# Performance work log

Measured on AMD Instinct MI355X. Metric: run time of the kernel, lower is better.

Reference implementation:

```python
import jax, jax.numpy as jnp
import numpy as np

B, L, C = 8, 3136, 192
HEADS, HEAD_CH = 3, 64
EPS = 1e-5


def _dwconv(x, w, s):
    # depthwise 3x3 conv, SAME padding; w: [3,3,1,C], feature_group_count=C
    return jax.lax.conv_general_dilated(
        x, w, (s, s), 'SAME',
        dimension_numbers=('NHWC', 'HWIO', 'NHWC'),
        feature_group_count=x.shape[-1])


def _proj(x, dw, scale, bias, mean, var, pw, s):
    # depthwise conv -> BN (inference, running stats) -> 1x1 pointwise conv
    h = _dwconv(x, dw, s)
    h = (h - mean) * jax.lax.rsqrt(var + EPS) * scale + bias
    return jax.lax.conv_general_dilated(
        h, pw, (1, 1), 'SAME',
        dimension_numbers=('NHWC', 'HWIO', 'NHWC'))


def setup_inputs() -> dict:
    key = jax.random.key(0)
    ks = jax.random.split(key, 7)
    d = {'x': jax.random.normal(ks[0], (B, L, C), jnp.float32)}
    for i, p in enumerate(['q', 'k', 'v']):
        d[p + '_dw'] = jax.random.normal(ks[i + 1], (3, 3, 1, C), jnp.float32) * 0.1
        d[p + '_scale'] = jnp.ones((C,), jnp.float32)
        d[p + '_bias'] = jnp.zeros((C,), jnp.float32)
        d[p + '_mean'] = jnp.zeros((C,), jnp.float32)
        d[p + '_var'] = jnp.ones((C,), jnp.float32)
        d[p + '_pw'] = jax.random.normal(ks[i + 4], (1, 1, C, HEADS * HEAD_CH), jnp.float32) * 0.05
    d['is_training'] = 0  # inference: BN uses running averages
    return d


def reference(x, q_dw, q_scale, q_bias, q_mean, q_var, q_pw,
              k_dw, k_scale, k_bias, k_mean, k_var, k_pw,
              v_dw, v_scale, v_bias, v_mean, v_var, v_pw,
              is_training):
    S = int(np.ceil(np.sqrt(L)))  # 56; L is a perfect square, so no token padding
    xi = x.reshape(B, S, S, C)
    q = _proj(xi, q_dw, q_scale, q_bias, q_mean, q_var, q_pw, 1)  # [B,56,56,192]
    k = _proj(xi, k_dw, k_scale, k_bias, k_mean, k_var, k_pw, 2)  # [B,28,28,192]
    v = _proj(xi, v_dw, v_scale, v_bias, v_mean, v_var, v_pw, 2)  # [B,28,28,192]
    q = q.reshape(B, -1, HEADS, HEAD_CH) / jnp.sqrt(jnp.float32(HEAD_CH))
    k = k.reshape(B, -1, HEADS, HEAD_CH)
    v = v.reshape(B, -1, HEADS, HEAD_CH)
    attn = jax.nn.softmax(jnp.einsum('bqhd,bkhd->bhqk', q, k), axis=-1)
    o = jnp.einsum('bhqk,bkhd->bqhd', attn, v)
    # num_heads*head_ch == out_ch -> plain head merge, no output projection
    return o.reshape(B, L, HEADS * HEAD_CH)
```

## Files before the change

### kernel.cpp

```cpp
#include <hip/hip_runtime.h>
#include <cmath>

#define EPS_BN 1e-5f

typedef __bf16 bf16;
typedef __bf16 bf16x4 __attribute__((ext_vector_type(4)));
typedef __bf16 bf16x8 __attribute__((ext_vector_type(8)));
typedef float  f32x4  __attribute__((ext_vector_type(4)));

__device__ __forceinline__ void dma16(const bf16* g, bf16* l) {
    __builtin_amdgcn_global_load_lds(
        (const __attribute__((address_space(1))) void*)g,
        (__attribute__((address_space(3))) void*)l, 16, 0, 0);
}

__device__ __forceinline__ float exp2_hw(float x) {
    float r;
    asm("v_exp_f32 %0, %1" : "=v"(r) : "v"(x));
    return r;
}

__global__ __launch_bounds__(256) void conv_all_kernel(
    const float* __restrict__ x,
    const float* __restrict__ qdw, const float* __restrict__ qscale,
    const float* __restrict__ qbias, const float* __restrict__ qmean,
    const float* __restrict__ qvar,
    const float* __restrict__ kdw, const float* __restrict__ kscale,
    const float* __restrict__ kbias, const float* __restrict__ kmean,
    const float* __restrict__ kvar,
    const float* __restrict__ vdw, const float* __restrict__ vscale,
    const float* __restrict__ vbias, const float* __restrict__ vmean,
    const float* __restrict__ vvar,
    const float* __restrict__ qpw, const float* __restrict__ kpw,
    const float* __restrict__ vpw,
    bf16* __restrict__ qhi, bf16* __restrict__ qlo,
    bf16* __restrict__ khi, bf16* __restrict__ klo,
    bf16* __restrict__ vhi, bf16* __restrict__ vlo,
    bf16* __restrict__ wt) {
    const int WW = 56, C = 192;
    int bid = blockIdx.x;

    if (bid < 4704) {
        int idx = bid * 256 + threadIdx.x;
        int p  = idx / 48;
        int c4 = (idx - p * 48) * 4;
        int b  = p / 3136;
        int rem = p - b * 3136;
        int oy = rem / 56;
        int ox = rem - oy * 56;
        const float* xb = x + (size_t)b * 3136 * C;

        float4 sc = *(const float4*)&qscale[c4];
        float4 vr = *(const float4*)&qvar[c4];
        float4 bi = *(const float4*)&qbias[c4];
        float4 mn = *(const float4*)&qmean[c4];
        float aA[4] = {sc.x * rsqrtf(vr.x + EPS_BN), sc.y * rsqrtf(vr.y + EPS_BN),
                       sc.z * rsqrtf(vr.z + EPS_BN), sc.w * rsqrtf(vr.w + EPS_BN)};
        float aB[4] = {bi.x - mn.x * aA[0], bi.y - mn.y * aA[1],
                       bi.z - mn.z * aA[2], bi.w - mn.w * aA[3]};
        float s[4] = {0.f, 0.f, 0.f, 0.f};
#pragma unroll
        for (int ky = 0; ky < 3; ky++) {
            int iy = oy + ky - 1;
            bool yok = (iy >= 0) && (iy < 56);
#pragma unroll
            for (int kx = 0; kx < 3; kx++) {
                int ix = ox + kx - 1;
                if (yok && ix >= 0 && ix < WW) {
                    float4 xv = *(const float4*)&xb[((size_t)iy * WW + ix) * C + c4];
                    float4 wv = *(const float4*)&qdw[(ky * 3 + kx) * C + c4];
                    s[0] += xv.x * wv.x; s[1] += xv.y * wv.y;
                    s[2] += xv.z * wv.z; s[3] += xv.w * wv.w;
                }
            }
        }
        bf16x4 hv, lv;
#pragma unroll
        for (int j = 0; j < 4; j++) {
            float av = s[j] * aA[j] + aB[j];
            bf16 hh = (bf16)av;
            hv[j] = hh;
            lv[j] = (bf16)(av - (float)hh);
        }
        *(bf16x4*)&qhi[(size_t)p * C + c4] = hv;
        *(bf16x4*)&qlo[(size_t)p * C + c4] = lv;
    } else if (bid < 5880) {
        int idx = (bid - 4704) * 256 + threadIdx.x;
        int p  = idx / 48;
        int c4 = (idx - p * 48) * 4;
        int b  = p / 784;
        int rem = p - b * 784;
        int oy = rem / 28;
        int ox = rem - oy * 28;
        const float* xb = x + (size_t)b * 3136 * C;

        float ks[4] = {0.f, 0.f, 0.f, 0.f};
        float vs[4] = {0.f, 0.f, 0.f, 0.f};
#pragma unroll
        for (int ky = 0; ky < 3; ky++) {
            int iy = oy * 2 + ky;
            bool yok = iy < 56;
#pragma unroll
            for (int kx = 0; kx < 3; kx++) {
                int ix = ox * 2 + kx;
                if (yok && ix < WW) {
                    float4 xv = *(const float4*)&xb[((size_t)iy * WW + ix) * C + c4];
                    float4 kw = *(const float4*)&kdw[(ky * 3 + kx) * C + c4];
                    float4 vw = *(const float4*)&vdw[(ky * 3 + kx) * C + c4];
                    ks[0] += xv.x * kw.x; ks[1] += xv.y * kw.y;
                    ks[2] += xv.z * kw.z; ks[3] += xv.w * kw.w;
                    vs[0] += xv.x * vw.x; vs[1] += xv.y * vw.y;
                    vs[2] += xv.z * vw.z; vs[3] += xv.w * vw.w;
                }
            }
        }
        float4 ksc = *(const float4*)&kscale[c4];
        float4 kvr = *(const float4*)&kvar[c4];
        float4 kbi = *(const float4*)&kbias[c4];
        float4 kmn = *(const float4*)&kmean[c4];
        float4 vsc = *(const float4*)&vscale[c4];
        float4 vvr = *(const float4*)&vvar[c4];
        float4 vbi = *(const float4*)&vbias[c4];
        float4 vmn = *(const float4*)&vmean[c4];
        float kA[4] = {ksc.x * rsqrtf(kvr.x + EPS_BN), ksc.y * rsqrtf(kvr.y + EPS_BN),
                       ksc.z * rsqrtf(kvr.z + EPS_BN), ksc.w * rsqrtf(kvr.w + EPS_BN)};
        float kB[4] = {kbi.x - kmn.x * kA[0], kbi.y - kmn.y * kA[1],
                       kbi.z - kmn.z * kA[2], kbi.w - kmn.w * kA[3]};
        float vA[4] = {vsc.x * rsqrtf(vvr.x + EPS_BN), vsc.y * rsqrtf(vvr.y + EPS_BN),
                       vsc.z * rsqrtf(vvr.z + EPS_BN), vsc.w * rsqrtf(vvr.w + EPS_BN)};
        float vB[4] = {vbi.x - vmn.x * vA[0], vbi.y - vmn.y * vA[1],
                       vbi.z - vmn.z * vA[2], vbi.w - vmn.w * vA[3]};
        bf16x4 kh, kl, vh, vl;
#pragma unroll
        for (int j = 0; j < 4; j++) {
            float kf = ks[j] * kA[j] + kB[j];
            float vf = vs[j] * vA[j] + vB[j];
            bf16 h1 = (bf16)kf; kh[j] = h1; kl[j] = (bf16)(kf - (float)h1);
            bf16 h2 = (bf16)vf; vh[j] = h2; vl[j] = (bf16)(vf - (float)h2);
        }
        *(bf16x4*)&khi[(size_t)p * C + c4] = kh;
        *(bf16x4*)&klo[(size_t)p * C + c4] = kl;
        *(bf16x4*)&vhi[(size_t)p * C + c4] = vh;
        *(bf16x4*)&vlo[(size_t)p * C + c4] = vl;
    } else {
        int idx = (bid - 5880) * 256 + threadIdx.x;
        if (idx < 3 * 36864) {
            int mat = idx / 36864, r = idx % 36864;
            int n = r / 192, k = r - n * 192;
            const float* src = (mat == 0) ? qpw : (mat == 1) ? kpw : vpw;
            wt[idx] = (bf16)src[k * 192 + n];
        }
    }
}

__global__ __launch_bounds__(256) void gemm_all_kernel(
    const bf16* __restrict__ qhi, const bf16* __restrict__ qlo,
    const bf16* __restrict__ khi, const bf16* __restrict__ klo,
    const bf16* __restrict__ vhi, const bf16* __restrict__ vlo,
    const bf16* __restrict__ wt,
    bf16* __restrict__ qbuf, bf16* __restrict__ kbuf, bf16* __restrict__ vtbuf) {
    __shared__ bf16 Ws[96][200];
    int t = threadIdx.x;
    int bid = blockIdx.x;

    int mode, mt, nh;
    const bf16 *Ahi, *Alo, *Wsrc;
    if (bid < 784)      { mode = 0; mt = bid >> 1;         nh = bid & 1;
                          Ahi = qhi; Alo = qlo; Wsrc = wt; }
    else if (bid < 980) { mode = 1; int r = bid - 784; mt = r >> 1; nh = r & 1;
                          Ahi = khi; Alo = klo; Wsrc = wt + 36864; }
    else                { mode = 2; int r = bid - 980; mt = r >> 1; nh = r & 1;
                          Ahi = vhi; Alo = vlo; Wsrc = wt + 73728; }
    int n0 = nh * 96;

#pragma unroll
    for (int it = 0; it < 9; it++) {
        int idx = it * 256 + t;
        int n = idx / 24, ck = idx - n * 24;
        *(uint4*)&Ws[n][ck * 8] = *(const uint4*)&Wsrc[(size_t)(n0 + n) * 192 + ck * 8];
    }
    __syncthreads();

    int lane = t & 63, wid = t >> 6;
    int l16 = lane & 15, quad = lane >> 4;
    int wrow = wid * 16;
    int m0 = mt * 64;

    f32x4 acc[6];
#pragma unroll
    for (int n = 0; n < 6; n++) acc[n] = f32x4{0.f, 0.f, 0.f, 0.f};

    const bf16* arh = Ahi + (size_t)(m0 + wrow + l16) * 192;
    const bf16* arl = Alo + (size_t)(m0 + wrow + l16) * 192;

    if (mode == 2) {
#pragma unroll
        for (int kc = 0; kc < 6; kc++) {
            bf16x8 ah = *(const bf16x8*)(arh + kc * 32 + quad * 8);
            bf16x8 al = *(const bf16x8*)(arl + kc * 32 + quad * 8);
#pragma unroll
            for (int n = 0; n < 6; n++) {
                bf16x8 bfr = *(const bf16x8*)&Ws[n * 16 + l16][kc * 32 + quad * 8];
                acc[n] = __builtin_amdgcn_mfma_f32_16x16x32_bf16(bfr, al, acc[n], 0, 0, 0);
                acc[n] = __builtin_amdgcn_mfma_f32_16x16x32_bf16(bfr, ah, acc[n], 0, 0, 0);
            }
        }
        int row = m0 + wrow + l16;
        int bb  = row / 784;
        int loc = row - bb * 784;
        bf16* vbase = vtbuf + (size_t)bb * 3 * 64 * 784 + loc;
#pragma unroll
        for (int n = 0; n < 6; n++)
#pragma unroll
            for (int reg = 0; reg < 4; reg++) {
                int col = n0 + n * 16 + quad * 4 + reg;
                int hh = col >> 6, d = col & 63;
                vbase[((size_t)hh * 64 + d) * 784] = (bf16)acc[n][reg];
            }
    } else {
#pragma unroll
        for (int kc = 0; kc < 6; kc++) {
            bf16x8 ah = *(const bf16x8*)(arh + kc * 32 + quad * 8);
            bf16x8 al = *(const bf16x8*)(arl + kc * 32 + quad * 8);
#pragma unroll
            for (int n = 0; n < 6; n++) {
                bf16x8 bfr = *(const bf16x8*)&Ws[n * 16 + l16][kc * 32 + quad * 8];
                acc[n] = __builtin_amdgcn_mfma_f32_16x16x32_bf16(al, bfr, acc[n], 0, 0, 0);
                acc[n] = __builtin_amdgcn_mfma_f32_16x16x32_bf16(ah, bfr, acc[n], 0, 0, 0);
            }
        }
        bf16* outp = (mode == 0) ? qbuf : kbuf;
        const float s = (mode == 0) ? 0.18033688f : 1.0f;
#pragma unroll
        for (int reg = 0; reg < 4; reg++) {
            size_t row = m0 + wrow + quad * 4 + reg;
#pragma unroll
            for (int n = 0; n < 6; n++)
                outp[row * 192 + n0 + n * 16 + l16] = (bf16)(acc[n][reg] * s);
        }
    }
}

__global__ __launch_bounds__(512)
__attribute__((amdgpu_waves_per_eu(4, 4)))
void attn3_kernel(const bf16* __restrict__ qb,
                  const bf16* __restrict__ kb,
                  const bf16* __restrict__ vtb,
                  float* __restrict__ out) {
    const int LQ = 3136, LK = 784, C = 192;
    int qt = blockIdx.x, h = blockIdx.y, b = blockIdx.z;

    __shared__ bf16 Ks[2][7168];
    __shared__ bf16 Vts[8192];
    __shared__ bf16 Ps[8192];

    int t    = threadIdx.x;
    int lane = t & 63;
    int wid  = t >> 6;
    int l16  = lane & 15;
    int quad = lane >> 4;
    int wrow = wid * 16;
    int l7   = l16 & 7;
    int qh   = quad >> 1;

    const bf16* kbase  = kb + (size_t)b * LK * C + h * 64;
    const bf16* vtbase = vtb + ((size_t)(b * 3 + h)) * 64 * LK;

    const bf16* ksrc = kbase + (lane >> 3) * C + (((lane & 7) ^ (lane >> 3)) * 8);

    int voff[2];
#pragma unroll
    for (int i = 0; i < 2; i++) {
        int s = wid + 8 * i;
        int j = s * 64 + lane;
        int row = j >> 4;
        int l = (j & 15) ^ (row & 7);
        voff[i] = row * LK + l * 8;
    }

    for (int s = wid; s < 14; s += 8)
        dma16(ksrc + s * 8 * C, &Ks[0][s * 512]);

    bf16x8 qfrag[2];
    {
        const bf16* qrow = qb + ((size_t)b * LQ + qt * 128 + wrow + l16) * C + h * 64;
        qfrag[0] = *(const bf16x8*)(qrow + quad * 8);
        qfrag[1] = *(const bf16x8*)(qrow + 32 + quad * 8);
    }
    bool qvalid = (qt < 24) || (wid < 4);

    int kA0 = l16 * 64 + (((quad    ) ^ l7) * 8);
    int kA1 = l16 * 64 + (((quad + 4) ^ l7) * 8);

    int prow   = (wrow + l16) * 64;
    int pwbase = prow + (quad & 1) * 4;

    float m_run = -INFINITY, l_run = 0.f;
    f32x4 o_acc[4];
#pragma unroll
    for (int dt = 0; dt < 4; dt++) o_acc[dt] = f32x4{0.f, 0.f, 0.f, 0.f};

    __syncthreads();

    for (int c = 0; c < 7; c++) {
        const int cur = c & 1, nxt = cur ^ 1;
        const int j0 = c * 112;

#pragma unroll
        for (int i = 0; i < 2; i++)
            dma16(vtbase + j0 + voff[i], Vts + (wid + 8 * i) * 512);
        __builtin_amdgcn_sched_barrier(0);

        if (c < 6) {
            const bf16* kn = ksrc + (size_t)(c + 1) * 112 * C;
            for (int s = wid; s < 14; s += 8)
                dma16(kn + s * 8 * C, &Ks[nxt][s * 512]);
        }
        __builtin_amdgcn_sched_barrier(0);

        f32x4 st[7];
#pragma unroll
        for (int kb7 = 0; kb7 < 7; kb7++) st[kb7] = f32x4{0.f, 0.f, 0.f, 0.f};
#pragma unroll
        for (int kk = 0; kk < 2; kk++) {
            int kA = (kk == 0) ? kA0 : kA1;
#pragma unroll
            for (int kb7 = 0; kb7 < 7; kb7++) {
                bf16x8 afrag = *(const bf16x8*)&Ks[cur][kb7 * 1024 + kA];
                st[kb7] = __builtin_amdgcn_mfma_f32_16x16x32_bf16(afrag, qfrag[kk], st[kb7], 0, 0, 0);
            }
        }

        float mx = -INFINITY;
#pragma unroll
        for (int kb7 = 0; kb7 < 7; kb7++)
#pragma unroll
            for (int r = 0; r < 4; r++) mx = fmaxf(mx, st[kb7][r]);
        mx = fmaxf(mx, __shfl_xor(mx, 16, 64));
        mx = fmaxf(mx, __shfl_xor(mx, 32, 64));

        bool defer = __all(mx - m_run <= 8.0f);
        float m_new = defer ? m_run : fmaxf(m_run, mx);

        float rs = 0.f;
        bf16x4 pk[7];
#pragma unroll
        for (int kb7 = 0; kb7 < 7; kb7++) {
            bf16x4 pv;
#pragma unroll
            for (int r = 0; r < 4; r++) {
                float p = exp2_hw(st[kb7][r] - m_new);
                rs += p;
                pv[r] = (bf16)p;
            }
            pk[kb7] = pv;
        }
        rs += __shfl_xor(rs, 16, 64);
        rs += __shfl_xor(rs, 32, 64);
        if (defer) {
            l_run += rs;
        } else {
            float alpha = exp2_hw(m_run - m_new);
            l_run = l_run * alpha + rs;
            m_run = m_new;
#pragma unroll
            for (int dt = 0; dt < 4; dt++)
#pragma unroll
                for (int r = 0; r < 4; r++) o_acc[dt][r] *= alpha;
        }

#pragma unroll
        for (int kb = 0; kb < 4; kb++)
            *(bf16x4*)&Ps[pwbase + (((kb * 2 + qh) ^ l7) * 8)] = pk[kb];

        if (c < 6) {
            if (wid < 6) asm volatile("s_waitcnt vmcnt(2)" ::: "memory");
            else         asm volatile("s_waitcnt vmcnt(1)" ::: "memory");
        } else {
            asm volatile("s_waitcnt vmcnt(0)" ::: "memory");
        }
        __builtin_amdgcn_s_barrier();
        __builtin_amdgcn_sched_barrier(0);

#pragma unroll
        for (int kk = 0; kk < 2; kk++) {
            bf16x8 pfrag = *(const bf16x8*)&Ps[prow + (((kk * 4 + quad) ^ l7) * 8)];
#pragma unroll
            for (int dt = 0; dt < 4; dt++) {
                bf16x8 vfrag = *(const bf16x8*)&Vts[(dt * 16 + l16) * 128
                                                   + (((kk * 4 + quad) ^ l7) * 8)];
                o_acc[dt] = __builtin_amdgcn_mfma_f32_16x16x32_bf16(vfrag, pfrag, o_acc[dt], 0, 0, 0);
            }
        }

#pragma unroll
        for (int kb = 0; kb < 3; kb++)
            *(bf16x4*)&Ps[pwbase + (((kb * 2 + qh) ^ l7) * 8)] = pk[4 + kb];
        {
            bf16x4 zv = {(bf16)0.f, (bf16)0.f, (bf16)0.f, (bf16)0.f};
            *(bf16x4*)&Ps[pwbase + (((6 + qh) ^ l7) * 8)] = zv;
        }

#pragma unroll
        for (int kk = 2; kk < 4; kk++) {
            bf16x8 pfrag = *(const bf16x8*)&Ps[prow + ((((kk - 2) * 4 + quad) ^ l7) * 8)];
#pragma unroll
            for (int dt = 0; dt < 4; dt++) {
                bf16x8 vfrag = *(const bf16x8*)&Vts[(dt * 16 + l16) * 128
                                                   + (((kk * 4 + quad) ^ l7) * 8)];
                o_acc[dt] = __builtin_amdgcn_mfma_f32_16x16x32_bf16(vfrag, pfrag, o_acc[dt], 0, 0, 0);
            }
        }

        __syncthreads();
    }

    if (qvalid) {
        float invl = 1.f / l_run;
        float* ob = out + ((size_t)b * LQ + qt * 128 + wrow + l16) * C + h * 64;
#pragma unroll
        for (int dt = 0; dt < 4; dt++) {
            float4 v4 = {o_acc[dt][0] * invl, o_acc[dt][1] * invl,
                         o_acc[dt][2] * invl, o_acc[dt][3] * invl};
            *(float4*)(ob + dt * 16 + quad * 4) = v4;
        }
    }
}

extern "C" void kernel_launch(void* const* d_in, const int* in_sizes, int n_in,
                              void* d_out, int out_size, void* d_ws, size_t ws_size,
                              hipStream_t stream) {
    const float* x = (const float*)d_in[0];

    const float* q_dw = (const float*)d_in[1];
    const float* q_scale = (const float*)d_in[2];
    const float* q_bias = (const float*)d_in[3];
    const float* q_mean = (const float*)d_in[4];
    const float* q_var = (const float*)d_in[5];
    const float* q_pw = (const float*)d_in[6];

    const float* k_dw = (const float*)d_in[7];
    const float* k_scale = (const float*)d_in[8];
    const float* k_bias = (const float*)d_in[9];
    const float* k_mean = (const float*)d_in[10];
    const float* k_var = (const float*)d_in[11];
    const float* k_pw = (const float*)d_in[12];

    const float* v_dw = (const float*)d_in[13];
    const float* v_scale = (const float*)d_in[14];
    const float* v_bias = (const float*)d_in[15];
    const float* v_mean = (const float*)d_in[16];
    const float* v_var = (const float*)d_in[17];
    const float* v_pw = (const float*)d_in[18];

    float* out = (float*)d_out;

    char* ws = (char*)d_ws;
    bf16* qhi = (bf16*)(ws);
    bf16* qlo = (bf16*)(ws + 9633792);
    bf16* khi = (bf16*)(ws + 19267584);
    bf16* klo = (bf16*)(ws + 21676032);
    bf16* vhi = (bf16*)(ws + 24084480);
    bf16* vlo = (bf16*)(ws + 26492928);
    bf16* qbuf = (bf16*)(ws + 28901376);
    bf16* kbuf = (bf16*)(ws + 38535168);
    bf16* vtbuf = (bf16*)(ws + 40943616);
    bf16* wt = (bf16*)(ws + 43352064);

    conv_all_kernel<<<6312, 256, 0, stream>>>(
        x,
        q_dw, q_scale, q_bias, q_mean, q_var,
        k_dw, k_scale, k_bias, k_mean, k_var,
        v_dw, v_scale, v_bias, v_mean, v_var,
        q_pw, k_pw, v_pw,
        qhi, qlo, khi, klo, vhi, vlo, wt);

    gemm_all_kernel<<<1176, 256, 0, stream>>>(
        qhi, qlo, khi, klo, vhi, vlo, wt, qbuf, kbuf, vtbuf);

    attn3_kernel<<<dim3(25, 3, 8), 512, 0, stream>>>(qbuf, kbuf, vtbuf, out);
}
```

Measured before the change: 174.2 us.

## Fuse Q depthwise conv, BN and pointwise GEMM into one kernel

The Q path's depthwise conv and BN now run in registers and feed the MFMA pointwise projection directly. The qhi/qlo intermediate buffers, about 19 MB written and read back, are no longer materialized. The fused kernel reads weights straight from global memory rather than LDS and uses only 392 blocks, so occupancy is low and the kernel may be latency bound. The conv and GEMM kernels shrink to the K/V work only.

```diff
diff --git a/kernel.cpp b/kernel.cpp
--- a/kernel.cpp
+++ b/kernel.cpp
@@ -22,9 +22,6 @@
 
 __global__ __launch_bounds__(256) void conv_all_kernel(
     const float* __restrict__ x,
-    const float* __restrict__ qdw, const float* __restrict__ qscale,
-    const float* __restrict__ qbias, const float* __restrict__ qmean,
-    const float* __restrict__ qvar,
     const float* __restrict__ kdw, const float* __restrict__ kscale,
     const float* __restrict__ kbias, const float* __restrict__ kmean,
     const float* __restrict__ kvar,
@@ -33,59 +30,14 @@
     const float* __restrict__ vvar,
     const float* __restrict__ qpw, const float* __restrict__ kpw,
     const float* __restrict__ vpw,
-    bf16* __restrict__ qhi, bf16* __restrict__ qlo,
     bf16* __restrict__ khi, bf16* __restrict__ klo,
     bf16* __restrict__ vhi, bf16* __restrict__ vlo,
     bf16* __restrict__ wt) {
     const int WW = 56, C = 192;
     int bid = blockIdx.x;
 
-    if (bid < 4704) {
+    if (bid < 1176) {
         int idx = bid * 256 + threadIdx.x;
-        int p  = idx / 48;
-        int c4 = (idx - p * 48) * 4;
-        int b  = p / 3136;
-        int rem = p - b * 3136;
-        int oy = rem / 56;
-        int ox = rem - oy * 56;
-        const float* xb = x + (size_t)b * 3136 * C;
-
-        float4 sc = *(const float4*)&qscale[c4];
-        float4 vr = *(const float4*)&qvar[c4];
-        float4 bi = *(const float4*)&qbias[c4];
-        float4 mn = *(const float4*)&qmean[c4];
-        float aA[4] = {sc.x * rsqrtf(vr.x + EPS_BN), sc.y * rsqrtf(vr.y + EPS_BN),
-                       sc.z * rsqrtf(vr.z + EPS_BN), sc.w * rsqrtf(vr.w + EPS_BN)};
-        float aB[4] = {bi.x - mn.x * aA[0], bi.y - mn.y * aA[1],
-                       bi.z - mn.z * aA[2], bi.w - mn.w * aA[3]};
-        float s[4] = {0.f, 0.f, 0.f, 0.f};
-#pragma unroll
-        for (int ky = 0; ky < 3; ky++) {
-            int iy = oy + ky - 1;
-            bool yok = (iy >= 0) && (iy < 56);
-#pragma unroll
-            for (int kx = 0; kx < 3; kx++) {
-                int ix = ox + kx - 1;
-                if (yok && ix >= 0 && ix < WW) {
-                    float4 xv = *(const float4*)&xb[((size_t)iy * WW + ix) * C + c4];
-                    float4 wv = *(const float4*)&qdw[(ky * 3 + kx) * C + c4];
-                    s[0] += xv.x * wv.x; s[1] += xv.y * wv.y;
-                    s[2] += xv.z * wv.z; s[3] += xv.w * wv.w;
-                }
-            }
-        }
-        bf16x4 hv, lv;
-#pragma unroll
-        for (int j = 0; j < 4; j++) {
-            float av = s[j] * aA[j] + aB[j];
-            bf16 hh = (bf16)av;
-            hv[j] = hh;
-            lv[j] = (bf16)(av - (float)hh);
-        }
-        *(bf16x4*)&qhi[(size_t)p * C + c4] = hv;
-        *(bf16x4*)&qlo[(size_t)p * C + c4] = lv;
-    } else if (bid < 5880) {
-        int idx = (bid - 4704) * 256 + threadIdx.x;
         int p  = idx / 48;
         int c4 = (idx - p * 48) * 4;
         int b  = p / 784;
@@ -143,7 +95,7 @@
         *(bf16x4*)&vhi[(size_t)p * C + c4] = vh;
         *(bf16x4*)&vlo[(size_t)p * C + c4] = vl;
     } else {
-        int idx = (bid - 5880) * 256 + threadIdx.x;
+        int idx = (bid - 1176) * 256 + threadIdx.x;
         if (idx < 3 * 36864) {
             int mat = idx / 36864, r = idx % 36864;
             int n = r / 192, k = r - n * 192;
@@ -153,24 +105,116 @@
     }
 }
 
+__global__ __launch_bounds__(256)
+__attribute__((amdgpu_waves_per_eu(3, 3)))
+void fusedq_kernel(const float* __restrict__ x,
+                   const float* __restrict__ qdw, const float* __restrict__ qscale,
+                   const float* __restrict__ qbias, const float* __restrict__ qmean,
+                   const float* __restrict__ qvar,
+                   const bf16* __restrict__ wt,
+                   bf16* __restrict__ qbuf) {
+    const int WW = 56, C = 192;
+    int t = threadIdx.x;
+    int lane = t & 63, wid = t >> 6;
+    int l16 = lane & 15, quad = lane >> 4;
+    int bid = blockIdx.x;
+    int b = bid / 49;
+    int p0 = (bid - b * 49) * 64;
+    int pix = p0 + wid * 16 + l16;
+    int oy = pix / 56, ox = pix - oy * 56;
+    const float* xb = x + (size_t)b * 3136 * C;
+
+    bf16x8 xhi[6], xlo[6];
+#pragma unroll
+    for (int kc = 0; kc < 6; kc++) {
+        int ch = kc * 32 + quad * 8;
+        float4 sc0 = *(const float4*)&qscale[ch],  sc1 = *(const float4*)&qscale[ch + 4];
+        float4 vr0 = *(const float4*)&qvar[ch],    vr1 = *(const float4*)&qvar[ch + 4];
+        float4 bi0 = *(const float4*)&qbias[ch],   bi1 = *(const float4*)&qbias[ch + 4];
+        float4 mn0 = *(const float4*)&qmean[ch],   mn1 = *(const float4*)&qmean[ch + 4];
+        float aA[8] = {sc0.x * rsqrtf(vr0.x + EPS_BN), sc0.y * rsqrtf(vr0.y + EPS_BN),
+                       sc0.z * rsqrtf(vr0.z + EPS_BN), sc0.w * rsqrtf(vr0.w + EPS_BN),
+                       sc1.x * rsqrtf(vr1.x + EPS_BN), sc1.y * rsqrtf(vr1.y + EPS_BN),
+                       sc1.z * rsqrtf(vr1.z + EPS_BN), sc1.w * rsqrtf(vr1.w + EPS_BN)};
+        float aB[8] = {bi0.x - mn0.x * aA[0], bi0.y - mn0.y * aA[1],
+                       bi0.z - mn0.z * aA[2], bi0.w - mn0.w * aA[3],
+                       bi1.x - mn1.x * aA[4], bi1.y - mn1.y * aA[5],
+                       bi1.z - mn1.z * aA[6], bi1.w - mn1.w * aA[7]};
+        float s[8] = {0.f, 0.f, 0.f, 0.f, 0.f, 0.f, 0.f, 0.f};
+#pragma unroll
+        for (int ky = 0; ky < 3; ky++) {
+            int iy = oy + ky - 1;
+            bool yok = (iy >= 0) && (iy < 56);
+#pragma unroll
+            for (int kx = 0; kx < 3; kx++) {
+                int ix = ox + kx - 1;
+                if (yok && ix >= 0 && ix < WW) {
+                    const float* xp = &xb[((size_t)iy * WW + ix) * C + ch];
+                    float4 xv0 = *(const float4*)xp;
+                    float4 xv1 = *(const float4*)(xp + 4);
+                    const float* wp = &qdw[(ky * 3 + kx) * C + ch];
+                    float4 wv0 = *(const float4*)wp;
+                    float4 wv1 = *(const float4*)(wp + 4);
+                    s[0] += xv0.x * wv0.x; s[1] += xv0.y * wv0.y;
+                    s[2] += xv0.z * wv0.z; s[3] += xv0.w * wv0.w;
+                    s[4] += xv1.x * wv1.x; s[5] += xv1.y * wv1.y;
+                    s[6] += xv1.z * wv1.z; s[7] += xv1.w * wv1.w;
+                }
+            }
+        }
+        bf16x8 hv, lv;
+#pragma unroll
+        for (int j = 0; j < 8; j++) {
+            float av = s[j] * aA[j] + aB[j];
+            bf16 hh = (bf16)av;
+            hv[j] = hh;
+            lv[j] = (bf16)(av - (float)hh);
+        }
+        xhi[kc] = hv;
+        xlo[kc] = lv;
+    }
+
+    f32x4 acc[12];
+#pragma unroll
+    for (int n = 0; n < 12; n++) acc[n] = f32x4{0.f, 0.f, 0.f, 0.f};
+
+    const bf16* wr = wt + (size_t)l16 * 192 + quad * 8;
+#pragma unroll
+    for (int kc = 0; kc < 6; kc++) {
+#pragma unroll
+        for (int nt = 0; nt < 12; nt++) {
+            bf16x8 w = *(const bf16x8*)(wr + nt * 3072 + kc * 32);
+            acc[nt] = __builtin_amdgcn_mfma_f32_16x16x32_bf16(w, xlo[kc], acc[nt], 0, 0, 0);
+            acc[nt] = __builtin_amdgcn_mfma_f32_16x16x32_bf16(w, xhi[kc], acc[nt], 0, 0, 0);
+        }
+    }
+
+    bf16* qp = qbuf + ((size_t)b * 3136 + pix) * 192 + quad * 4;
+#pragma unroll
+    for (int nt = 0; nt < 12; nt++) {
+        bf16x4 ov;
+#pragma unroll
+        for (int reg = 0; reg < 4; reg++)
+            ov[reg] = (bf16)(acc[nt][reg] * 0.18033688f);
+        *(bf16x4*)(qp + nt * 16) = ov;
+    }
+}
+
 __global__ __launch_bounds__(256) void gemm_all_kernel(
-    const bf16* __restrict__ qhi, const bf16* __restrict__ qlo,
     const bf16* __restrict__ khi, const bf16* __restrict__ klo,
     const bf16* __restrict__ vhi, const bf16* __restrict__ vlo,
     const bf16* __restrict__ wt,
-    bf16* __restrict__ qbuf, bf16* __restrict__ kbuf, bf16* __restrict__ vtbuf) {
+    bf16* __restrict__ kbuf, bf16* __restrict__ vtbuf) {
     __shared__ bf16 Ws[96][200];
     int t = threadIdx.x;
     int bid = blockIdx.x;
 
     int mode, mt, nh;
     const bf16 *Ahi, *Alo, *Wsrc;
-    if (bid < 784)      { mode = 0; mt = bid >> 1;         nh = bid & 1;
-                          Ahi = qhi; Alo = qlo; Wsrc = wt; }
-    else if (bid < 980) { mode = 1; int r = bid - 784; mt = r >> 1; nh = r & 1;
-                          Ahi = khi; Alo = klo; Wsrc = wt + 36864; }
-    else                { mode = 2; int r = bid - 980; mt = r >> 1; nh = r & 1;
-                          Ahi = vhi; Alo = vlo; Wsrc = wt + 73728; }
+    if (bid < 196) { mode = 1; mt = bid >> 1; nh = bid & 1;
+                     Ahi = khi; Alo = klo; Wsrc = wt + 36864; }
+    else           { mode = 2; int r = bid - 196; mt = r >> 1; nh = r & 1;
+                     Ahi = vhi; Alo = vlo; Wsrc = wt + 73728; }
     int n0 = nh * 96;
 
 #pragma unroll
@@ -229,14 +273,12 @@
                 acc[n] = __builtin_amdgcn_mfma_f32_16x16x32_bf16(ah, bfr, acc[n], 0, 0, 0);
             }
         }
-        bf16* outp = (mode == 0) ? qbuf : kbuf;
-        const float s = (mode == 0) ? 0.18033688f : 1.0f;
 #pragma unroll
         for (int reg = 0; reg < 4; reg++) {
             size_t row = m0 + wrow + quad * 4 + reg;
 #pragma unroll
             for (int n = 0; n < 6; n++)
-                outp[row * 192 + n0 + n * 16 + l16] = (bf16)(acc[n][reg] * s);
+                kbuf[row * 192 + n0 + n * 16 + l16] = (bf16)acc[n][reg];
         }
     }
 }
@@ -456,8 +498,6 @@
     float* out = (float*)d_out;
 
     char* ws = (char*)d_ws;
-    bf16* qhi = (bf16*)(ws);
-    bf16* qlo = (bf16*)(ws + 9633792);
     bf16* khi = (bf16*)(ws + 19267584);
     bf16* klo = (bf16*)(ws + 21676032);
     bf16* vhi = (bf16*)(ws + 24084480);
@@ -467,16 +507,18 @@
     bf16* vtbuf = (bf16*)(ws + 40943616);
     bf16* wt = (bf16*)(ws + 43352064);
 
-    conv_all_kernel<<<6312, 256, 0, stream>>>(
+    conv_all_kernel<<<1608, 256, 0, stream>>>(
         x,
-        q_dw, q_scale, q_bias, q_mean, q_var,
         k_dw, k_scale, k_bias, k_mean, k_var,
         v_dw, v_scale, v_bias, v_mean, v_var,
         q_pw, k_pw, v_pw,
-        qhi, qlo, khi, klo, vhi, vlo, wt);
-
-    gemm_all_kernel<<<1176, 256, 0, stream>>>(
-        qhi, qlo, khi, klo, vhi, vlo, wt, qbuf, kbuf, vtbuf);
+        khi, klo, vhi, vlo, wt);
+
+    fusedq_kernel<<<392, 256, 0, stream>>>(
+        x, q_dw, q_scale, q_bias, q_mean, q_var, wt, qbuf);
+
+    gemm_all_kernel<<<392, 256, 0, stream>>>(
+        khi, klo, vhi, vlo, wt, kbuf, vtbuf);
 
     attn3_kernel<<<dim3(25, 3, 8), 512, 0, stream>>>(qbuf, kbuf, vtbuf, out);
 }
```

Measured after the change: 218.4 us. +25.4%, slower.
